# Performance work log

Measured on AMD Instinct MI355X. Metric: run time of the kernel, lower is better.

The kernel has to match this reference:

```python
import jax, jax.numpy as jnp
import numpy as np

N, D, H = 4096, 2048, 16
DK = D // H  # 128


def setup_inputs() -> dict:
    key = jax.random.key(0)
    k0, k1, k2, k3 = jax.random.split(key, 4)
    return {
        "tokens_embedding": jax.random.normal(k0, (N, D), dtype=jnp.float32),
        "w_q": jax.random.normal(k1, (H, D, DK), dtype=jnp.float32),
        "w_k": jax.random.normal(k2, (H, D, DK), dtype=jnp.float32),
        "w_v": jax.random.normal(k3, (H, D, DK), dtype=jnp.float32),
    }


def reference(tokens_embedding, w_q, w_k, w_v):
    # Per-head projections (batched over heads): [H, N, DK]
    q = jnp.einsum('nd,hdk->hnk', tokens_embedding, w_q)
    k = jnp.einsum('nd,hdk->hnk', tokens_embedding, w_k)
    v = jnp.einsum('nd,hdk->hnk', tokens_embedding, w_v)
    # Scaled dot-product attention, softmax over keys (orig dim=1 of [N,N])
    scale = 1.0 / jnp.sqrt(jnp.float32(DK))
    scores = jnp.einsum('hnk,hmk->hnm', q, k) * scale  # [H, N, N]
    attn = jax.nn.softmax(scores, axis=-1)
    out = jnp.einsum('hnm,hmk->hnk', attn, v)  # [H, N, DK]
    # Concat heads along feature dim (head order preserved): [N, H*DK]
    return jnp.transpose(out, (1, 0, 2)).reshape(N, H * DK)
```

## Files before the change

kernel.cpp:

```cpp
#include <hip/hip_runtime.h>
#include <hip/hip_bf16.h>

#define N_TOK 4096
#define D_MODEL 2048
#define NHEAD 16
#define DKH 128

typedef __attribute__((ext_vector_type(8))) short short8v;
typedef __attribute__((ext_vector_type(4))) float f32x4;
typedef __attribute__((ext_vector_type(4))) unsigned short ush4;
typedef __attribute__((ext_vector_type(8))) unsigned short ush8;

static __device__ __forceinline__ unsigned short f2bf(float f) {
  unsigned int x = __float_as_uint(f);
  return (unsigned short)((x + 0x7fffu + ((x >> 16) & 1u)) >> 16);
}
static __device__ __forceinline__ float bf2f(unsigned short u) {
  return __uint_as_float(((unsigned int)u) << 16);
}

static __device__ __forceinline__ void gld16(const void* g, void* l) {
  __builtin_amdgcn_global_load_lds(
      (const __attribute__((address_space(1))) unsigned int*)g,
      (__attribute__((address_space(3))) unsigned int*)l, 16, 0, 0);
}

__global__ __launch_bounds__(256)
void split_e_kernel(const float* __restrict__ E,
                    unsigned short* __restrict__ Eh,
                    unsigned short* __restrict__ El) {
  const size_t i = ((size_t)blockIdx.x * 256 + threadIdx.x) * 8;
  const int n = (int)(i >> 11), d0 = (int)(i & 2047);
  float4 v0 = *reinterpret_cast<const float4*>(E + i);
  float4 v1 = *reinterpret_cast<const float4*>(E + i + 4);
  float f[8] = {v0.x, v0.y, v0.z, v0.w, v1.x, v1.y, v1.z, v1.w};
  ush8 hi, lo;
#pragma unroll
  for (int j = 0; j < 8; ++j) {
    unsigned short hu = f2bf(f[j]);
    hi[j] = hu;
    lo[j] = f2bf(f[j] - bf2f(hu));
  }
  const size_t off = (size_t)n * D_MODEL + (d0 ^ ((n & 7) << 3));
  *reinterpret_cast<ush8*>(Eh + off) = hi;
  *reinterpret_cast<ush8*>(El + off) = lo;
}

__global__ __launch_bounds__(256)
void split_w_kernel(const float* __restrict__ Wq, const float* __restrict__ Wk,
                    const float* __restrict__ Wv,
                    unsigned short* __restrict__ WTh,
                    unsigned short* __restrict__ WTl) {
  __shared__ float tile[64][65];
  const int t = threadIdx.x;
  const int d0 = blockIdx.x * 64;
  const int k0 = blockIdx.y * 64;
  const int mh = blockIdx.z;
  const int mat = mh >> 4, h = mh & 15;
  const float* W = (mat == 0) ? Wq : (mat == 1) ? Wk : Wv;
  const float* Wp = W + (size_t)h * D_MODEL * DKH;
  const float fac = (mat == 0) ? (1.44269504089f / sqrtf(128.0f)) : 1.0f;

  const int rr = t >> 4, c4 = (t & 15) * 4;
#pragma unroll
  for (int p = 0; p < 4; ++p) {
    float4 v = *reinterpret_cast<const float4*>(Wp + (size_t)(d0 + rr + 16 * p) * DKH + k0 + c4);
    tile[rr + 16 * p][c4 + 0] = v.x * fac;
    tile[rr + 16 * p][c4 + 1] = v.y * fac;
    tile[rr + 16 * p][c4 + 2] = v.z * fac;
    tile[rr + 16 * p][c4 + 3] = v.w * fac;
  }
  __syncthreads();
  const int dd0 = (t & 7) * 8, kl = t >> 3;
#pragma unroll
  for (int p = 0; p < 2; ++p) {
    const int kg = k0 + kl + 32 * p;
    ush8 hi, lo;
#pragma unroll
    for (int j = 0; j < 8; ++j) {
      float f = tile[dd0 + j][kl + 32 * p];
      unsigned short hu = f2bf(f);
      hi[j] = hu;
      lo[j] = f2bf(f - bf2f(hu));
    }
    const size_t base = ((size_t)(mat * NHEAD + h) * DKH + kg) * D_MODEL +
                        d0 + (dd0 ^ ((kg & 7) << 3));
    *reinterpret_cast<ush8*>(WTh + base) = hi;
    if (mat < 2) *reinterpret_cast<ush8*>(WTl + base) = lo;
  }
}

template <int MODE>
__global__ __launch_bounds__(256, 2)
void proj_gemm_kernel(const unsigned short* __restrict__ Eh,
                      const unsigned short* __restrict__ El,
                      const unsigned short* __restrict__ WTh,
                      const unsigned short* __restrict__ WTl,
                      unsigned short* __restrict__ Qhi, unsigned short* __restrict__ Qlo,
                      unsigned short* __restrict__ Khi, unsigned short* __restrict__ Klo,
                      unsigned short* __restrict__ Vt, int h0) {
  __shared__ alignas(16) unsigned short Ah[128 * 64];
  __shared__ alignas(16) unsigned short Bh[128 * 64];
  __shared__ alignas(16) unsigned short Al[MODE == 0 ? 128 * 64 : 16];
  __shared__ alignas(16) unsigned short Bl[MODE == 0 ? 128 * 64 : 16];

  const int t = threadIdx.x;
  const int nb = blockIdx.x, hl = blockIdx.y, h = h0 + hl;
  const int mat = (MODE == 0) ? blockIdx.z : 2;
  const int wv = t >> 6, lane = t & 63, fr = lane & 15, fq = lane >> 4;
  const int m0 = (wv >> 1) * 64, n0 = (wv & 1) * 64;

  const char *pAh, *pBh, *pAl = nullptr, *pBl = nullptr;
  if (MODE == 0) {
    pAh = (const char*)(Eh + (size_t)nb * 128 * D_MODEL);
    pAl = (const char*)(El + (size_t)nb * 128 * D_MODEL);
    pBh = (const char*)(WTh + ((size_t)mat * NHEAD + h) * DKH * D_MODEL);
    pBl = (const char*)(WTl + ((size_t)mat * NHEAD + h) * DKH * D_MODEL);
  } else {
    pAh = (const char*)(WTh + ((size_t)2 * NHEAD + h) * DKH * D_MODEL);
    pBh = (const char*)(Eh + (size_t)nb * 128 * D_MODEL);
  }

  f32x4 acc[4][4];
#pragma unroll
  for (int a = 0; a < 4; ++a)
#pragma unroll
    for (int b = 0; b < 4; ++b) acc[a][b] = f32x4{0.f, 0.f, 0.f, 0.f};

  for (int d0 = 0; d0 < D_MODEL; d0 += 64) {
    __syncthreads();
    {
      const size_t gb = (size_t)d0 * 2 + (size_t)(t >> 3) * 4096 + (t & 7) * 16;
#pragma unroll
      for (int j = 0; j < 4; ++j) {
        gld16(pAh + gb + (size_t)j * 32 * 4096, (char*)Ah + j * 4096 + t * 16);
        gld16(pBh + gb + (size_t)j * 32 * 4096, (char*)Bh + j * 4096 + t * 16);
      }
      if (MODE == 0) {
#pragma unroll
        for (int j = 0; j < 4; ++j) {
          gld16(pAl + gb + (size_t)j * 32 * 4096, (char*)Al + j * 4096 + t * 16);
          gld16(pBl + gb + (size_t)j * 32 * 4096, (char*)Bl + j * 4096 + t * 16);
        }
      }
    }
    __syncthreads();
    __builtin_amdgcn_s_setprio(1);
#pragma unroll
    for (int ks = 0; ks < 2; ++ks) {
      short8v ah[4], al[4];
#pragma unroll
      for (int mi = 0; mi < 4; ++mi) {
        const int r = m0 + 16 * mi + fr;
        const int off = (ks * 32 + fq * 8) ^ ((r & 7) << 3);
        ah[mi] = *reinterpret_cast<const short8v*>(&Ah[r * 64 + off]);
        if (MODE == 0) al[mi] = *reinterpret_cast<const short8v*>(&Al[r * 64 + off]);
      }
#pragma unroll
      for (int ni = 0; ni < 4; ++ni) {
        const int rn = n0 + 16 * ni + fr;
        const int offn = (ks * 32 + fq * 8) ^ ((rn & 7) << 3);
        short8v bh = *reinterpret_cast<const short8v*>(&Bh[rn * 64 + offn]);
        if (MODE == 0) {
          short8v bl = *reinterpret_cast<const short8v*>(&Bl[rn * 64 + offn]);
#pragma unroll
          for (int mi = 0; mi < 4; ++mi) {
            acc[mi][ni] = __builtin_amdgcn_mfma_f32_16x16x32_bf16(ah[mi], bh, acc[mi][ni], 0, 0, 0);
            acc[mi][ni] = __builtin_amdgcn_mfma_f32_16x16x32_bf16(ah[mi], bl, acc[mi][ni], 0, 0, 0);
            acc[mi][ni] = __builtin_amdgcn_mfma_f32_16x16x32_bf16(al[mi], bh, acc[mi][ni], 0, 0, 0);
          }
        } else {
#pragma unroll
          for (int mi = 0; mi < 4; ++mi)
            acc[mi][ni] = __builtin_amdgcn_mfma_f32_16x16x32_bf16(ah[mi], bh, acc[mi][ni], 0, 0, 0);
        }
      }
    }
    __builtin_amdgcn_s_setprio(0);
  }

  if (MODE == 0) {
    unsigned short* Ohi = (mat == 0) ? Qhi : Khi;
    unsigned short* Olo = (mat == 0) ? Qlo : Klo;
#pragma unroll
    for (int mi = 0; mi < 4; ++mi)
#pragma unroll
      for (int ni = 0; ni < 4; ++ni)
#pragma unroll
        for (int i = 0; i < 4; ++i) {
          float v = acc[mi][ni][i];
          unsigned short hu = f2bf(v);
          unsigned short lu = f2bf(v - bf2f(hu));
          int n = nb * 128 + m0 + 16 * mi + fq * 4 + i;
          int k = n0 + 16 * ni + fr;
          if (mat == 1) k ^= ((n & 7) << 3);
          size_t off = ((size_t)hl * N_TOK + n) * DKH + k;
          Ohi[off] = hu;
          Olo[off] = lu;
        }
  } else {
#pragma unroll
    for (int mi = 0; mi < 4; ++mi)
#pragma unroll
      for (int ni = 0; ni < 4; ++ni)
#pragma unroll
        for (int i = 0; i < 4; ++i) {
          int kout = m0 + 16 * mi + fq * 4 + i;
          int tn = nb * 128 + n0 + 16 * ni + fr;
          int ts = (tn & ~63) | ((tn & 63) ^ ((kout & 7) << 3));
          Vt[((size_t)hl * DKH + kout) * N_TOK + ts] = f2bf(acc[mi][ni][i]);
        }
  }
}

__global__ __launch_bounds__(256, 2)
void attn_kernel(const unsigned short* __restrict__ Qhi,
                 const unsigned short* __restrict__ Qlo,
                 const unsigned short* __restrict__ Khi,
                 const unsigned short* __restrict__ Klo,
                 const unsigned short* __restrict__ Vt,
                 float* __restrict__ out, int h0, int HC)
{
  __shared__ alignas(16) unsigned short KhiL[64][128];
  __shared__ alignas(16) unsigned short KloL[64][128];
  __shared__ alignas(16) unsigned short VtL[128][64];
  __shared__ unsigned int PL32[4][2][32][20];

  const int t = threadIdx.x;
  int b = blockIdx.x;
  const int nwg = 32 * HC;
  if ((nwg & 7) == 0) b = (b & 7) * (nwg >> 3) + (b >> 3);
  const int qb = b & 31;
  const int hl = b >> 5;
  const int h  = h0 + hl;
  const int wv = t >> 6, lane = t & 63;
  const int fr = lane & 15, fq = lane >> 4;
  const int q0 = qb * 128 + wv * 32;

  short8v qhi[2][4], qlo[2][4];
#pragma unroll
  for (int m = 0; m < 2; ++m) {
    const unsigned short* qp  = Qhi + ((size_t)hl * N_TOK + q0 + m * 16 + fr) * DKH + fq * 8;
    const unsigned short* qp2 = Qlo + ((size_t)hl * N_TOK + q0 + m * 16 + fr) * DKH + fq * 8;
#pragma unroll
    for (int kc = 0; kc < 4; ++kc) {
      qhi[m][kc] = *reinterpret_cast<const short8v*>(qp + kc * 32);
      qlo[m][kc] = *reinterpret_cast<const short8v*>(qp2 + kc * 32);
    }
  }

  f32x4 o[2][8];
#pragma unroll
  for (int m = 0; m < 2; ++m)
#pragma unroll
    for (int i = 0; i < 8; ++i) o[m][i] = f32x4{0.f, 0.f, 0.f, 0.f};
  float mrow[2] = {-__builtin_inff(), -__builtin_inff()};
  float lrow[2] = {0.f, 0.f};

  const char* KhiB = (const char*)(Khi + (size_t)hl * N_TOK * DKH);
  const char* KloB = (const char*)(Klo + (size_t)hl * N_TOK * DKH);
  const char* VtB  = (const char*)(Vt  + (size_t)hl * DKH * N_TOK);
  const int toff = t * 16;
  const int vrow = t >> 3, vbyte = (t & 7) * 16;

  for (int kt = 0; kt < N_TOK / 64; ++kt) {
    const int key0 = kt * 64;
    __syncthreads();
    {
      const char* gk  = KhiB + (size_t)key0 * 256;
      const char* gk2 = KloB + (size_t)key0 * 256;
#pragma unroll
      for (int j = 0; j < 4; ++j)
        gld16(gk + j * 4096 + toff, (char*)&KhiL[0][0] + j * 4096 + toff);
#pragma unroll
      for (int j = 0; j < 4; ++j)
        gld16(gk2 + j * 4096 + toff, (char*)&KloL[0][0] + j * 4096 + toff);
#pragma unroll
      for (int j = 0; j < 4; ++j)
        gld16(VtB + (size_t)(j * 32 + vrow) * (N_TOK * 2) + key0 * 2 + vbyte,
              (char*)&VtL[0][0] + j * 4096 + toff);
    }
    __syncthreads();

    f32x4 tt[2][4];
#pragma unroll
    for (int m = 0; m < 2; ++m)
#pragma unroll
      for (int kf = 0; kf < 4; ++kf) tt[m][kf] = f32x4{0.f, 0.f, 0.f, 0.f};
    __builtin_amdgcn_s_setprio(1);
#pragma unroll
    for (int kc = 0; kc < 4; ++kc) {
      short8v khf[4], klf[4];
#pragma unroll
      for (int kf = 0; kf < 4; ++kf) {
        const int kr = kf * 16 + fr;
        const int off = (kc * 32 + fq * 8) ^ ((kr & 7) << 3);
        khf[kf] = *reinterpret_cast<const short8v*>(&KhiL[kr][off]);
        klf[kf] = *reinterpret_cast<const short8v*>(&KloL[kr][off]);
      }
#pragma unroll
      for (int kf = 0; kf < 4; ++kf)
#pragma unroll
        for (int m = 0; m < 2; ++m) {
          tt[m][kf] = __builtin_amdgcn_mfma_f32_16x16x32_bf16(khf[kf], qhi[m][kc], tt[m][kf], 0, 0, 0);
          tt[m][kf] = __builtin_amdgcn_mfma_f32_16x16x32_bf16(klf[kf], qhi[m][kc], tt[m][kf], 0, 0, 0);
          tt[m][kf] = __builtin_amdgcn_mfma_f32_16x16x32_bf16(khf[kf], qlo[m][kc], tt[m][kf], 0, 0, 0);
        }
    }
    __builtin_amdgcn_s_setprio(0);

    float mx[2];
#pragma unroll
    for (int m = 0; m < 2; ++m) {
      float v = -__builtin_inff();
#pragma unroll
      for (int kf = 0; kf < 4; ++kf)
#pragma unroll
        for (int i = 0; i < 4; ++i) v = fmaxf(v, tt[m][kf][i]);
      v = fmaxf(v, __shfl_xor(v, 16));
      v = fmaxf(v, __shfl_xor(v, 32));
      mx[m] = v;
    }
    if (__any((mx[0] > mrow[0]) | (mx[1] > mrow[1]))) {
#pragma unroll
      for (int m = 0; m < 2; ++m) {
        float mn = fmaxf(mrow[m], mx[m]);
        float al = exp2f(mrow[m] - mn);
        mrow[m] = mn;
        lrow[m] *= al;
#pragma unroll
        for (int of = 0; of < 8; ++of)
#pragma unroll
          for (int i = 0; i < 4; ++i) o[m][of][i] *= al;
      }
    }
#pragma unroll
    for (int m = 0; m < 2; ++m) {
      float rs = 0.f;
#pragma unroll
      for (int kf = 0; kf < 4; ++kf)
#pragma unroll
        for (int hh = 0; hh < 2; ++hh) {
          float p0 = exp2f(tt[m][kf][2 * hh]     - mrow[m]);
          float p1 = exp2f(tt[m][kf][2 * hh + 1] - mrow[m]);
          unsigned short b0 = f2bf(p0), b1 = f2bf(p1);
          rs += bf2f(b0) + bf2f(b1);
          PL32[wv][m][kf * 8 + 2 * fq + hh][fr] = (unsigned)b0 | ((unsigned)b1 << 16);
        }
      rs += __shfl_xor(rs, 16);
      rs += __shfl_xor(rs, 32);
      lrow[m] += rs;
    }
    asm volatile("s_waitcnt lgkmcnt(0)" ::: "memory");
    __builtin_amdgcn_sched_barrier(0);

    __builtin_amdgcn_s_setprio(1);
#pragma unroll
    for (int ks = 0; ks < 2; ++ks) {
      union { unsigned u[4]; short8v v; } pb[2];
#pragma unroll
      for (int m = 0; m < 2; ++m)
#pragma unroll
        for (int w = 0; w < 4; ++w)
          pb[m].u[w] = PL32[wv][m][16 * ks + 4 * fq + w][fr];
#pragma unroll
      for (int of = 0; of < 8; ++of) {
        const int dr = of * 16 + fr;
        short8v av = *reinterpret_cast<const short8v*>(
            &VtL[dr][(ks * 32 + fq * 8) ^ ((dr & 7) << 3)]);
#pragma unroll
        for (int m = 0; m < 2; ++m)
          o[m][of] = __builtin_amdgcn_mfma_f32_16x16x32_bf16(av, pb[m].v, o[m][of], 0, 0, 0);
      }
    }
    __builtin_amdgcn_s_setprio(0);
  }

#pragma unroll
  for (int m = 0; m < 2; ++m) {
    float inv = 1.0f / lrow[m];
    int n = q0 + m * 16 + fr;
    float* op = out + (size_t)n * (NHEAD * DKH) + h * DKH + fq * 4;
#pragma unroll
    for (int of = 0; of < 8; ++of) {
      float4 r = make_float4(o[m][of][0] * inv, o[m][of][1] * inv,
                             o[m][of][2] * inv, o[m][of][3] * inv);
      *reinterpret_cast<float4*>(op + of * 16) = r;
    }
  }
}

extern "C" void kernel_launch(void* const* d_in, const int* in_sizes, int n_in,
                              void* d_out, int out_size, void* d_ws, size_t ws_size,
                              hipStream_t stream) {
  (void)in_sizes; (void)n_in; (void)out_size;
  const float* E  = (const float*)d_in[0];
  const float* Wq = (const float*)d_in[1];
  const float* Wk = (const float*)d_in[2];
  const float* Wv = (const float*)d_in[3];
  float* out = (float*)d_out;

  const size_t ND   = (size_t)N_TOK * D_MODEL;
  const size_t WThE = (size_t)3 * NHEAD * DKH * D_MODEL;
  const size_t WTlE = (size_t)2 * NHEAD * DKH * D_MODEL;
  const size_t phe  = (size_t)N_TOK * DKH;
  const size_t baseE = 2 * ND + WThE + WTlE;

  unsigned short* Eh  = (unsigned short*)d_ws;
  unsigned short* El  = Eh + ND;
  unsigned short* WTh = El + ND;
  unsigned short* WTl = WTh + WThE;
  unsigned short* chunk = WTl + WTlE;

  int HC = NHEAD;
  while (HC > 1 && (baseE + (size_t)HC * 5 * phe) * 2 > ws_size) HC >>= 1;

  split_e_kernel<<<dim3((unsigned)(ND / 8 / 256)), 256, 0, stream>>>(E, Eh, El);
  split_w_kernel<<<dim3(32, 2, 48), 256, 0, stream>>>(Wq, Wk, Wv, WTh, WTl);

  for (int h0 = 0; h0 < NHEAD; h0 += HC) {
    unsigned short* Qhi = chunk;
    unsigned short* Qlo = Qhi + (size_t)HC * phe;
    unsigned short* Khi = Qlo + (size_t)HC * phe;
    unsigned short* Klo = Khi + (size_t)HC * phe;
    unsigned short* Vt  = Klo + (size_t)HC * phe;
    proj_gemm_kernel<1><<<dim3(32, HC, 1), 256, 0, stream>>>(Eh, El, WTh, WTl,
                                                             Qhi, Qlo, Khi, Klo, Vt, h0);
    proj_gemm_kernel<0><<<dim3(32, HC, 2), 256, 0, stream>>>(Eh, El, WTh, WTl,
                                                             Qhi, Qlo, Khi, Klo, Vt, h0);
    attn_kernel<<<dim3(32 * HC), 256, 0, stream>>>(Qhi, Qlo, Khi, Klo, Vt, out, h0, HC);
  }
}
```

Before: 500.3 us.

## Pre-tile E and W into MFMA fragment layout and load directly to registers

The split kernels now write the bf16 hi/lo copies of E and W into a fragment-major layout that matches the MFMA operand order. The projection GEMM then drops the LDS staging and its barriers, loading fragments straight from global memory into registers with a two-stage software prefetch. The grid is flattened and remapped with an XCD-style interleave. Each wave re-reads operands from global/L2 instead of sharing them through LDS, which raises cache traffic and register pressure, and the occupancy hint was removed.

Result: slower. 574.4 us (+14.8%).

```diff
diff --git a/kernel.cpp b/kernel.cpp
--- a/kernel.cpp
+++ b/kernel.cpp
@@ -8,7 +8,6 @@
 
 typedef __attribute__((ext_vector_type(8))) short short8v;
 typedef __attribute__((ext_vector_type(4))) float f32x4;
-typedef __attribute__((ext_vector_type(4))) unsigned short ush4;
 typedef __attribute__((ext_vector_type(8))) unsigned short ush8;
 
 static __device__ __forceinline__ unsigned short f2bf(float f) {
@@ -24,6 +23,7 @@
       (const __attribute__((address_space(1))) unsigned int*)g,
       (__attribute__((address_space(3))) unsigned int*)l, 16, 0, 0);
 }
+
 
 __global__ __launch_bounds__(256)
 void split_e_kernel(const float* __restrict__ E,
@@ -41,7 +41,9 @@
     hi[j] = hu;
     lo[j] = f2bf(f[j] - bf2f(hu));
   }
-  const size_t off = (size_t)n * D_MODEL + (d0 ^ ((n & 7) << 3));
+  const int nb = n >> 7, mt = (n >> 4) & 7, fr = n & 15;
+  const int kidx = d0 >> 5, fq = (d0 >> 3) & 3;
+  const size_t off = ((((size_t)nb * 64 + kidx) * 8 + mt) * 64 + fq * 16 + fr) * 8;
   *reinterpret_cast<ush8*>(Eh + off) = hi;
   *reinterpret_cast<ush8*>(El + off) = lo;
 }
@@ -49,8 +51,8 @@
 __global__ __launch_bounds__(256)
 void split_w_kernel(const float* __restrict__ Wq, const float* __restrict__ Wk,
                     const float* __restrict__ Wv,
-                    unsigned short* __restrict__ WTh,
-                    unsigned short* __restrict__ WTl) {
+                    unsigned short* __restrict__ WBh,
+                    unsigned short* __restrict__ WBl) {
   __shared__ float tile[64][65];
   const int t = threadIdx.x;
   const int d0 = blockIdx.x * 64;
@@ -72,9 +74,11 @@
   }
   __syncthreads();
   const int dd0 = (t & 7) * 8, kl = t >> 3;
+  const int kidx = ((d0 + dd0) >> 5), fq = (dd0 >> 3) & 3;
 #pragma unroll
   for (int p = 0; p < 2; ++p) {
     const int kg = k0 + kl + 32 * p;
+    const int nt = kg >> 4, fr = kg & 15;
     ush8 hi, lo;
 #pragma unroll
     for (int j = 0; j < 8; ++j) {
@@ -83,43 +87,53 @@
       hi[j] = hu;
       lo[j] = f2bf(f - bf2f(hu));
     }
-    const size_t base = ((size_t)(mat * NHEAD + h) * DKH + kg) * D_MODEL +
-                        d0 + (dd0 ^ ((kg & 7) << 3));
-    *reinterpret_cast<ush8*>(WTh + base) = hi;
-    if (mat < 2) *reinterpret_cast<ush8*>(WTl + base) = lo;
+    const size_t dst = ((((size_t)mh * 64 + kidx) * 8 + nt) * 64 + fq * 16 + fr) * 8;
+    *reinterpret_cast<ush8*>(WBh + dst) = hi;
+    if (mat < 2) *reinterpret_cast<ush8*>(WBl + dst) = lo;
   }
 }
 
 template <int MODE>
-__global__ __launch_bounds__(256, 2)
-void proj_gemm_kernel(const unsigned short* __restrict__ Eh,
-                      const unsigned short* __restrict__ El,
-                      const unsigned short* __restrict__ WTh,
-                      const unsigned short* __restrict__ WTl,
-                      unsigned short* __restrict__ Qhi, unsigned short* __restrict__ Qlo,
-                      unsigned short* __restrict__ Khi, unsigned short* __restrict__ Klo,
-                      unsigned short* __restrict__ Vt, int h0) {
-  __shared__ alignas(16) unsigned short Ah[128 * 64];
-  __shared__ alignas(16) unsigned short Bh[128 * 64];
-  __shared__ alignas(16) unsigned short Al[MODE == 0 ? 128 * 64 : 16];
-  __shared__ alignas(16) unsigned short Bl[MODE == 0 ? 128 * 64 : 16];
-
+__global__ __launch_bounds__(256)
+void proj2_kernel(const unsigned short* __restrict__ EhF,
+                  const unsigned short* __restrict__ ElF,
+                  const unsigned short* __restrict__ WBh,
+                  const unsigned short* __restrict__ WBl,
+                  unsigned short* __restrict__ Qhi, unsigned short* __restrict__ Qlo,
+                  unsigned short* __restrict__ Khi, unsigned short* __restrict__ Klo,
+                  unsigned short* __restrict__ Vt, int h0, int HC) {
+  int id = blockIdx.x;
+  const int nwg = gridDim.x;
+  id = (id & 7) * (nwg >> 3) + (id >> 3);
+  int nb, hl, mat;
+  if (MODE == 0) {
+    const int hm2 = id % (2 * HC);
+    nb = id / (2 * HC);
+    mat = hm2 & 1;
+    hl = hm2 >> 1;
+  } else {
+    nb = id / HC;
+    hl = id % HC;
+    mat = 2;
+  }
+  const int h = h0 + hl;
   const int t = threadIdx.x;
-  const int nb = blockIdx.x, hl = blockIdx.y, h = h0 + hl;
-  const int mat = (MODE == 0) ? blockIdx.z : 2;
   const int wv = t >> 6, lane = t & 63, fr = lane & 15, fq = lane >> 4;
   const int m0 = (wv >> 1) * 64, n0 = (wv & 1) * 64;
 
-  const char *pAh, *pBh, *pAl = nullptr, *pBl = nullptr;
+  constexpr int NF = (MODE == 0) ? 8 : 4;
+  const unsigned short *Ab, *Al = nullptr, *Bb, *Bl = nullptr;
   if (MODE == 0) {
-    pAh = (const char*)(Eh + (size_t)nb * 128 * D_MODEL);
-    pAl = (const char*)(El + (size_t)nb * 128 * D_MODEL);
-    pBh = (const char*)(WTh + ((size_t)mat * NHEAD + h) * DKH * D_MODEL);
-    pBl = (const char*)(WTl + ((size_t)mat * NHEAD + h) * DKH * D_MODEL);
+    Ab = EhF + (size_t)nb * 64 * 4096 + lane * 8;
+    Al = ElF + (size_t)nb * 64 * 4096 + lane * 8;
+    const size_t wb = (size_t)(mat * NHEAD + h) * 64 * 4096;
+    Bb = WBh + wb + lane * 8;
+    Bl = WBl + wb + lane * 8;
   } else {
-    pAh = (const char*)(WTh + ((size_t)2 * NHEAD + h) * DKH * D_MODEL);
-    pBh = (const char*)(Eh + (size_t)nb * 128 * D_MODEL);
-  }
+    Ab = WBh + (size_t)(2 * NHEAD + h) * 64 * 4096 + lane * 8;
+    Bb = EhF + (size_t)nb * 64 * 4096 + lane * 8;
+  }
+  const int ta = m0 >> 4, tb = n0 >> 4;
 
   f32x4 acc[4][4];
 #pragma unroll
@@ -127,56 +141,38 @@
 #pragma unroll
     for (int b = 0; b < 4; ++b) acc[a][b] = f32x4{0.f, 0.f, 0.f, 0.f};
 
-  for (int d0 = 0; d0 < D_MODEL; d0 += 64) {
-    __syncthreads();
-    {
-      const size_t gb = (size_t)d0 * 2 + (size_t)(t >> 3) * 4096 + (t & 7) * 16;
-#pragma unroll
-      for (int j = 0; j < 4; ++j) {
-        gld16(pAh + gb + (size_t)j * 32 * 4096, (char*)Ah + j * 4096 + t * 16);
-        gld16(pBh + gb + (size_t)j * 32 * 4096, (char*)Bh + j * 4096 + t * 16);
+  auto loadf = [&](short8v* A, short8v* B, int kidx) {
+    const size_t ko = (size_t)kidx * 4096;
+#pragma unroll
+    for (int i = 0; i < 4; ++i) {
+      A[i] = *reinterpret_cast<const short8v*>(Ab + ko + (ta + i) * 512);
+      B[i] = *reinterpret_cast<const short8v*>(Bb + ko + (tb + i) * 512);
+      if (MODE == 0) {
+        A[4 + i] = *reinterpret_cast<const short8v*>(Al + ko + (ta + i) * 512);
+        B[4 + i] = *reinterpret_cast<const short8v*>(Bl + ko + (tb + i) * 512);
       }
-      if (MODE == 0) {
-#pragma unroll
-        for (int j = 0; j < 4; ++j) {
-          gld16(pAl + gb + (size_t)j * 32 * 4096, (char*)Al + j * 4096 + t * 16);
-          gld16(pBl + gb + (size_t)j * 32 * 4096, (char*)Bl + j * 4096 + t * 16);
+    }
+  };
+  auto mfmas = [&](const short8v* A, const short8v* B) {
+#pragma unroll
+    for (int ni = 0; ni < 4; ++ni)
+#pragma unroll
+      for (int mi = 0; mi < 4; ++mi) {
+        acc[mi][ni] = __builtin_amdgcn_mfma_f32_16x16x32_bf16(A[mi], B[ni], acc[mi][ni], 0, 0, 0);
+        if (MODE == 0) {
+          acc[mi][ni] = __builtin_amdgcn_mfma_f32_16x16x32_bf16(A[mi], B[4 + ni], acc[mi][ni], 0, 0, 0);
+          acc[mi][ni] = __builtin_amdgcn_mfma_f32_16x16x32_bf16(A[4 + mi], B[ni], acc[mi][ni], 0, 0, 0);
         }
       }
-    }
-    __syncthreads();
-    __builtin_amdgcn_s_setprio(1);
-#pragma unroll
-    for (int ks = 0; ks < 2; ++ks) {
-      short8v ah[4], al[4];
-#pragma unroll
-      for (int mi = 0; mi < 4; ++mi) {
-        const int r = m0 + 16 * mi + fr;
-        const int off = (ks * 32 + fq * 8) ^ ((r & 7) << 3);
-        ah[mi] = *reinterpret_cast<const short8v*>(&Ah[r * 64 + off]);
-        if (MODE == 0) al[mi] = *reinterpret_cast<const short8v*>(&Al[r * 64 + off]);
-      }
-#pragma unroll
-      for (int ni = 0; ni < 4; ++ni) {
-        const int rn = n0 + 16 * ni + fr;
-        const int offn = (ks * 32 + fq * 8) ^ ((rn & 7) << 3);
-        short8v bh = *reinterpret_cast<const short8v*>(&Bh[rn * 64 + offn]);
-        if (MODE == 0) {
-          short8v bl = *reinterpret_cast<const short8v*>(&Bl[rn * 64 + offn]);
-#pragma unroll
-          for (int mi = 0; mi < 4; ++mi) {
-            acc[mi][ni] = __builtin_amdgcn_mfma_f32_16x16x32_bf16(ah[mi], bh, acc[mi][ni], 0, 0, 0);
-            acc[mi][ni] = __builtin_amdgcn_mfma_f32_16x16x32_bf16(ah[mi], bl, acc[mi][ni], 0, 0, 0);
-            acc[mi][ni] = __builtin_amdgcn_mfma_f32_16x16x32_bf16(al[mi], bh, acc[mi][ni], 0, 0, 0);
-          }
-        } else {
-#pragma unroll
-          for (int mi = 0; mi < 4; ++mi)
-            acc[mi][ni] = __builtin_amdgcn_mfma_f32_16x16x32_bf16(ah[mi], bh, acc[mi][ni], 0, 0, 0);
-        }
-      }
-    }
-    __builtin_amdgcn_s_setprio(0);
+  };
+
+  short8v aP[NF], bP[NF], aQ[NF], bQ[NF];
+  loadf(aP, bP, 0);
+  for (int k2 = 0; k2 < 64; k2 += 2) {
+    loadf(aQ, bQ, k2 + 1);
+    mfmas(aP, bP);
+    if (k2 + 2 < 64) loadf(aP, bP, k2 + 2);
+    mfmas(aQ, bQ);
   }
 
   if (MODE == 0) {
@@ -408,15 +404,15 @@
 
   unsigned short* Eh  = (unsigned short*)d_ws;
   unsigned short* El  = Eh + ND;
-  unsigned short* WTh = El + ND;
-  unsigned short* WTl = WTh + WThE;
-  unsigned short* chunk = WTl + WTlE;
+  unsigned short* WBh = El + ND;
+  unsigned short* WBl = WBh + WThE;
+  unsigned short* chunk = WBl + WTlE;
 
   int HC = NHEAD;
   while (HC > 1 && (baseE + (size_t)HC * 5 * phe) * 2 > ws_size) HC >>= 1;
 
   split_e_kernel<<<dim3((unsigned)(ND / 8 / 256)), 256, 0, stream>>>(E, Eh, El);
-  split_w_kernel<<<dim3(32, 2, 48), 256, 0, stream>>>(Wq, Wk, Wv, WTh, WTl);
+  split_w_kernel<<<dim3(32, 2, 48), 256, 0, stream>>>(Wq, Wk, Wv, WBh, WBl);
 
   for (int h0 = 0; h0 < NHEAD; h0 += HC) {
     unsigned short* Qhi = chunk;
@@ -424,10 +420,10 @@
     unsigned short* Khi = Qlo + (size_t)HC * phe;
     unsigned short* Klo = Khi + (size_t)HC * phe;
     unsigned short* Vt  = Klo + (size_t)HC * phe;
-    proj_gemm_kernel<1><<<dim3(32, HC, 1), 256, 0, stream>>>(Eh, El, WTh, WTl,
-                                                             Qhi, Qlo, Khi, Klo, Vt, h0);
-    proj_gemm_kernel<0><<<dim3(32, HC, 2), 256, 0, stream>>>(Eh, El, WTh, WTl,
-                                                             Qhi, Qlo, Khi, Klo, Vt, h0);
+    proj2_kernel<1><<<dim3(32 * HC), 256, 0, stream>>>(Eh, El, WBh, WBl,
+                                                       Qhi, Qlo, Khi, Klo, Vt, h0, HC);
+    proj2_kernel<0><<<dim3(32 * 2 * HC), 256, 0, stream>>>(Eh, El, WBh, WBl,
+                                                           Qhi, Qlo, Khi, Klo, Vt, h0, HC);
     attn_kernel<<<dim3(32 * HC), 256, 0, stream>>>(Qhi, Qlo, Khi, Klo, Vt, out, h0, HC);
   }
 }
```

## Double-buffer 32-key tiles and pass P via ds_bpermute instead of LDS

Applied to the files above, without the earlier changes.

The attention loop now stages 32-key tiles of K hi/lo and V into double-buffered LDS, so the next tile's global-to-LDS loads are issued before the current tile is computed. This is meant to hide load latency behind compute. The probability fragment is moved between lanes with ds_bpermute instead of a round trip through an LDS scratch array. V is rewritten into a tiled, swizzled layout so that each tile is one contiguous 8KB copy. Tiles are half as large, so there are twice as many barriers per key range, and the hand-set vmcnt count must match the number of loads per stage.

After: 538.9 us. 1.08x slower.

```diff
diff --git a/kernel.cpp b/kernel.cpp
--- a/kernel.cpp
+++ b/kernel.cpp
@@ -8,7 +8,6 @@
 
 typedef __attribute__((ext_vector_type(8))) short short8v;
 typedef __attribute__((ext_vector_type(4))) float f32x4;
-typedef __attribute__((ext_vector_type(4))) unsigned short ush4;
 typedef __attribute__((ext_vector_type(8))) unsigned short ush8;
 
 static __device__ __forceinline__ unsigned short f2bf(float f) {
@@ -207,8 +206,10 @@
         for (int i = 0; i < 4; ++i) {
           int kout = m0 + 16 * mi + fq * 4 + i;
           int tn = nb * 128 + n0 + 16 * ni + fr;
-          int ts = (tn & ~63) | ((tn & 63) ^ ((kout & 7) << 3));
-          Vt[((size_t)hl * DKH + kout) * N_TOK + ts] = f2bf(acc[mi][ni][i]);
+          int tile = tn >> 5, key = tn & 31;
+          int L = ((kout >> 1) << 6) + ((kout & 1) << 5) +
+                  ((((key >> 3) ^ ((kout >> 1) & 3))) << 3) + (key & 7);
+          Vt[((size_t)hl * 128 + tile) * 4096 + L] = f2bf(acc[mi][ni][i]);
         }
   }
 }
@@ -221,10 +222,9 @@
                  const unsigned short* __restrict__ Vt,
                  float* __restrict__ out, int h0, int HC)
 {
-  __shared__ alignas(16) unsigned short KhiL[64][128];
-  __shared__ alignas(16) unsigned short KloL[64][128];
-  __shared__ alignas(16) unsigned short VtL[128][64];
-  __shared__ unsigned int PL32[4][2][32][20];
+  __shared__ alignas(16) unsigned short KhiL[2][32][128];
+  __shared__ alignas(16) unsigned short KloL[2][32][128];
+  __shared__ alignas(16) unsigned short VtL[2][4096];
 
   const int t = threadIdx.x;
   int b = blockIdx.x;
@@ -259,47 +259,42 @@
 
   const char* KhiB = (const char*)(Khi + (size_t)hl * N_TOK * DKH);
   const char* KloB = (const char*)(Klo + (size_t)hl * N_TOK * DKH);
-  const char* VtB  = (const char*)(Vt  + (size_t)hl * DKH * N_TOK);
+  const char* VtB  = (const char*)(Vt  + (size_t)hl * (size_t)N_TOK * DKH);
   const int toff = t * 16;
-  const int vrow = t >> 3, vbyte = (t & 7) * 16;
-
-  for (int kt = 0; kt < N_TOK / 64; ++kt) {
-    const int key0 = kt * 64;
-    __syncthreads();
-    {
-      const char* gk  = KhiB + (size_t)key0 * 256;
-      const char* gk2 = KloB + (size_t)key0 * 256;
-#pragma unroll
-      for (int j = 0; j < 4; ++j)
-        gld16(gk + j * 4096 + toff, (char*)&KhiL[0][0] + j * 4096 + toff);
-#pragma unroll
-      for (int j = 0; j < 4; ++j)
-        gld16(gk2 + j * 4096 + toff, (char*)&KloL[0][0] + j * 4096 + toff);
-#pragma unroll
-      for (int j = 0; j < 4; ++j)
-        gld16(VtB + (size_t)(j * 32 + vrow) * (N_TOK * 2) + key0 * 2 + vbyte,
-              (char*)&VtL[0][0] + j * 4096 + toff);
-    }
-    __syncthreads();
-
-    f32x4 tt[2][4];
+  const int ga0 = (fr + ((fq & 1) << 5)) << 2;
+  const int ga1 = ga0 + 64;
+
+  auto stage = [&](int tile, int buf) {
+    const char* gk  = KhiB + (size_t)tile * 8192;
+    const char* gk2 = KloB + (size_t)tile * 8192;
+    const char* gv  = VtB  + (size_t)tile * 8192;
+#pragma unroll
+    for (int j = 0; j < 2; ++j) {
+      gld16(gk  + j * 4096 + toff, (char*)&KhiL[buf][0][0] + j * 4096 + toff);
+      gld16(gk2 + j * 4096 + toff, (char*)&KloL[buf][0][0] + j * 4096 + toff);
+      gld16(gv  + j * 4096 + toff, (char*)&VtL[buf][0]     + j * 4096 + toff);
+    }
+  };
+
+  auto compute = [&](int cur) {
+    f32x4 tt[2][2];
 #pragma unroll
     for (int m = 0; m < 2; ++m)
 #pragma unroll
-      for (int kf = 0; kf < 4; ++kf) tt[m][kf] = f32x4{0.f, 0.f, 0.f, 0.f};
+      for (int kf = 0; kf < 2; ++kf) tt[m][kf] = f32x4{0.f, 0.f, 0.f, 0.f};
     __builtin_amdgcn_s_setprio(1);
 #pragma unroll
     for (int kc = 0; kc < 4; ++kc) {
-      short8v khf[4], klf[4];
-#pragma unroll
-      for (int kf = 0; kf < 4; ++kf) {
+      short8v khf[2], klf[2];
+#pragma unroll
+      for (int kf = 0; kf < 2; ++kf) {
         const int kr = kf * 16 + fr;
         const int off = (kc * 32 + fq * 8) ^ ((kr & 7) << 3);
-        khf[kf] = *reinterpret_cast<const short8v*>(&KhiL[kr][off]);
-        klf[kf] = *reinterpret_cast<const short8v*>(&KloL[kr][off]);
-      }
-#pragma unroll
-      for (int kf = 0; kf < 4; ++kf)
+        khf[kf] = *reinterpret_cast<const short8v*>(&KhiL[cur][kr][off]);
+        klf[kf] = *reinterpret_cast<const short8v*>(&KloL[cur][kr][off]);
+      }
+#pragma unroll
+      for (int kf = 0; kf < 2; ++kf)
 #pragma unroll
         for (int m = 0; m < 2; ++m) {
           tt[m][kf] = __builtin_amdgcn_mfma_f32_16x16x32_bf16(khf[kf], qhi[m][kc], tt[m][kf], 0, 0, 0);
@@ -312,11 +307,8 @@
     float mx[2];
 #pragma unroll
     for (int m = 0; m < 2; ++m) {
-      float v = -__builtin_inff();
-#pragma unroll
-      for (int kf = 0; kf < 4; ++kf)
-#pragma unroll
-        for (int i = 0; i < 4; ++i) v = fmaxf(v, tt[m][kf][i]);
+      float v = fmaxf(fmaxf(fmaxf(tt[m][0][0], tt[m][0][1]), fmaxf(tt[m][0][2], tt[m][0][3])),
+                      fmaxf(fmaxf(tt[m][1][0], tt[m][1][1]), fmaxf(tt[m][1][2], tt[m][1][3])));
       v = fmaxf(v, __shfl_xor(v, 16));
       v = fmaxf(v, __shfl_xor(v, 32));
       mx[m] = v;
@@ -334,47 +326,72 @@
           for (int i = 0; i < 4; ++i) o[m][of][i] *= al;
       }
     }
+    unsigned pp[2][2][2];
 #pragma unroll
     for (int m = 0; m < 2; ++m) {
       float rs = 0.f;
 #pragma unroll
-      for (int kf = 0; kf < 4; ++kf)
+      for (int kf = 0; kf < 2; ++kf)
 #pragma unroll
         for (int hh = 0; hh < 2; ++hh) {
           float p0 = exp2f(tt[m][kf][2 * hh]     - mrow[m]);
           float p1 = exp2f(tt[m][kf][2 * hh + 1] - mrow[m]);
           unsigned short b0 = f2bf(p0), b1 = f2bf(p1);
           rs += bf2f(b0) + bf2f(b1);
-          PL32[wv][m][kf * 8 + 2 * fq + hh][fr] = (unsigned)b0 | ((unsigned)b1 << 16);
+          pp[m][kf][hh] = (unsigned)b0 | ((unsigned)b1 << 16);
         }
       rs += __shfl_xor(rs, 16);
       rs += __shfl_xor(rs, 32);
       lrow[m] += rs;
     }
-    asm volatile("s_waitcnt lgkmcnt(0)" ::: "memory");
+
+    union { unsigned u[4]; short8v v; } pb[2];
+#pragma unroll
+    for (int m = 0; m < 2; ++m) {
+      unsigned c00 = __builtin_amdgcn_ds_bpermute(ga0, pp[m][0][0]);
+      unsigned c10 = __builtin_amdgcn_ds_bpermute(ga0, pp[m][1][0]);
+      unsigned c01 = __builtin_amdgcn_ds_bpermute(ga0, pp[m][0][1]);
+      unsigned c11 = __builtin_amdgcn_ds_bpermute(ga0, pp[m][1][1]);
+      unsigned d00 = __builtin_amdgcn_ds_bpermute(ga1, pp[m][0][0]);
+      unsigned d10 = __builtin_amdgcn_ds_bpermute(ga1, pp[m][1][0]);
+      unsigned d01 = __builtin_amdgcn_ds_bpermute(ga1, pp[m][0][1]);
+      unsigned d11 = __builtin_amdgcn_ds_bpermute(ga1, pp[m][1][1]);
+      const bool hi = (fq & 2);
+      pb[m].u[0] = hi ? c10 : c00;
+      pb[m].u[1] = hi ? c11 : c01;
+      pb[m].u[2] = hi ? d10 : d00;
+      pb[m].u[3] = hi ? d11 : d01;
+    }
+
+    __builtin_amdgcn_s_setprio(1);
+#pragma unroll
+    for (int of = 0; of < 8; ++of) {
+      const int dr = of * 16 + fr;
+      const char* vp = (const char*)&VtL[cur][0] +
+                       (dr >> 1) * 128 + (dr & 1) * 64 + ((fq ^ ((dr >> 1) & 3)) << 4);
+      short8v av = *reinterpret_cast<const short8v*>(vp);
+#pragma unroll
+      for (int m = 0; m < 2; ++m)
+        o[m][of] = __builtin_amdgcn_mfma_f32_16x16x32_bf16(av, pb[m].v, o[m][of], 0, 0, 0);
+    }
+    __builtin_amdgcn_s_setprio(0);
+  };
+
+  stage(0, 0);
+  asm volatile("s_waitcnt vmcnt(0)" ::: "memory");
+  __builtin_amdgcn_s_barrier();
+  for (int tile = 0; tile < 127; ++tile) {
+    stage(tile + 1, (tile + 1) & 1);
+    asm volatile("s_waitcnt vmcnt(6)" ::: "memory");
+    __builtin_amdgcn_s_barrier();
     __builtin_amdgcn_sched_barrier(0);
-
-    __builtin_amdgcn_s_setprio(1);
-#pragma unroll
-    for (int ks = 0; ks < 2; ++ks) {
-      union { unsigned u[4]; short8v v; } pb[2];
-#pragma unroll
-      for (int m = 0; m < 2; ++m)
-#pragma unroll
-        for (int w = 0; w < 4; ++w)
-          pb[m].u[w] = PL32[wv][m][16 * ks + 4 * fq + w][fr];
-#pragma unroll
-      for (int of = 0; of < 8; ++of) {
-        const int dr = of * 16 + fr;
-        short8v av = *reinterpret_cast<const short8v*>(
-            &VtL[dr][(ks * 32 + fq * 8) ^ ((dr & 7) << 3)]);
-#pragma unroll
-        for (int m = 0; m < 2; ++m)
-          o[m][of] = __builtin_amdgcn_mfma_f32_16x16x32_bf16(av, pb[m].v, o[m][of], 0, 0, 0);
-      }
-    }
-    __builtin_amdgcn_s_setprio(0);
-  }
+    compute(tile & 1);
+    __builtin_amdgcn_sched_barrier(0);
+    __builtin_amdgcn_s_barrier();
+  }
+  asm volatile("s_waitcnt vmcnt(0)" ::: "memory");
+  __builtin_amdgcn_s_barrier();
+  compute(1);
 
 #pragma unroll
   for (int m = 0; m < 2; ++m) {
```
